# Kernel tuning notes

Measured on AMD Instinct MI355X. Metric: run time of the kernel, lower is better.

Reference implementation:

```python
import jax, jax.numpy as jnp
import numpy as np
import math

B, T, E, F, K, NUM_CONV, H = 32, 2048, 512, 512, 7, 4, 8
EPS = 1e-5


def _ln2(x):
    # fresh nn.LayerNorm(x.size()[1:]): normalize jointly over last two dims, weight=1 bias=0
    mu = jnp.mean(x, axis=(-2, -1), keepdims=True)
    var = jnp.var(x, axis=(-2, -1), keepdims=True)
    return (x - mu) * jax.lax.rsqrt(var + EPS)


def _ds_conv(x, dw_w, dw_b, pw_w, pw_b):
    # x: (B, C, T); depthwise conv (groups=C) then pointwise 1x1
    C = x.shape[1]
    k = dw_w.shape[-1]
    y = jax.lax.conv_general_dilated(
        x, dw_w, window_strides=(1,), padding=[(k // 2, k // 2)],
        dimension_numbers=('NCH', 'OIH', 'NCH'), feature_group_count=C)
    y = y + dw_b[None, :, None]
    y = jnp.einsum('oc,bct->bot', pw_w, y) + pw_b[None, :, None]
    return y


def _pos_enc(n, e):
    # pe[i, 0::2] = sin(i * div), pe[i, 1::2] = cos(i * div); returns (n, 1, e)
    pos = jnp.arange(n, dtype=jnp.float32)[:, None]
    div = jnp.exp(jnp.arange(0, e, 2, dtype=jnp.float32) * (-math.log(10000.0) / e))
    pe = jnp.zeros((n, e), dtype=jnp.float32)
    pe = pe.at[:, 0::2].set(jnp.sin(pos * div)).at[:, 1::2].set(jnp.cos(pos * div))
    return pe[:, None, :]


def setup_inputs() -> dict:
    key = jax.random.key(0)
    ks = jax.random.split(key, 20)
    w = lambda i, shape: (jax.random.normal(ks[i], shape, jnp.float32) * 0.02)
    return {
        'x': jax.random.normal(ks[0], (B, T, E), jnp.float32),
        'dw1_w': w(1, (E, 1, K)), 'dw1_b': w(2, (E,)),
        'pw1_w': w(3, (F, E)), 'pw1_b': w(4, (F,)),
        'dw2_w': w(5, (F, 1, K)), 'dw2_b': w(6, (F,)),
        'pw2_w': w(7, (F, F)), 'pw2_b': w(8, (F,)),
        'wq': w(9, (F, F)), 'bq': w(10, (F,)),
        'wk': w(11, (F, F)), 'bk': w(12, (F,)),
        'wv': w(13, (F, F)), 'bv': w(14, (F,)),
        'wp': w(15, (F, F)), 'bp': w(16, (F,)),
        'ff_w': w(17, (F, F)), 'ff_b': w(18, (F,)),
    }


def reference(x, dw1_w, dw1_b, pw1_w, pw1_b, dw2_w, dw2_b, pw2_w, pw2_b,
              wq, bq, wk, bk, wv, bv, wp, bp, ff_w, ff_b):
    b, t, e = x.shape
    # positional encoding: pe[:x.size(0)] -> (B,1,E), broadcast over T (faithful quirk)
    x = x + _pos_enc(b, e)
    x = jnp.transpose(x, (0, 2, 1))          # (B, E, T)
    x = _ln2(x)
    x = _ds_conv(x, dw1_w, dw1_b, pw1_w, pw1_b)   # (B, F, T)
    for _ in range(NUM_CONV - 1):                 # shared conv weights each iter (faithful)
        x = x + _ds_conv(_ln2(x), dw2_w, dw2_b, pw2_w, pw2_b)
    # attention: code permutes to (T, B, F) so attention attends across the batch axis
    y = jnp.transpose(_ln2(x), (2, 0, 1))    # (T, B, F)
    x = jnp.transpose(x, (2, 0, 1))          # (T, B, F)
    f = x.shape[-1]
    hd = f // H
    q = (y @ wq.T + bq).reshape(t, b, H, hd).transpose(0, 2, 1, 3)  # (T, H, B, hd)
    k = (y @ wk.T + bk).reshape(t, b, H, hd).transpose(0, 2, 1, 3)
    v = (y @ wv.T + bv).reshape(t, b, H, hd).transpose(0, 2, 1, 3)
    att = jnp.einsum('thbd,thcd->thbc', q, k) * (1.0 / math.sqrt(hd))
    att = jax.nn.softmax(att, axis=-1)
    yo = jnp.einsum('thbc,thcd->thbd', att, v)
    yo = yo.transpose(0, 2, 1, 3).reshape(t, b, f)
    yo = yo @ wp.T + bp
    x = x + yo
    y = _ln2(x)                               # norm over last-two dims (B, F)
    y = y @ ff_w.T + ff_b
    x = x + y
    return jnp.transpose(x, (1, 0, 2))        # (B, T, F)
```

## Files before the change

### kernel.cpp

```cpp
#include <hip/hip_runtime.h>
#include <math.h>

constexpr int B_ = 32, T_ = 2048, E_ = 512, F_ = 512, KW = 7, H_ = 8;
constexpr float EPS_ = 1e-5f;

typedef unsigned short bfu;
typedef __attribute__((ext_vector_type(8))) unsigned short ushort8v;
typedef __attribute__((ext_vector_type(8))) short short8v;
typedef __attribute__((ext_vector_type(4))) float f32x4;
typedef const __attribute__((address_space(1))) void* gp1_t;
typedef __attribute__((address_space(3))) void* lp3_t;

__device__ __forceinline__ float b2f(bfu u) {
    return __uint_as_float(((unsigned)u) << 16);
}
__device__ __forceinline__ bfu f2b(float f) {
    unsigned i = __float_as_uint(f);
    i += 0x7fffu + ((i >> 16) & 1u);
    return (bfu)(i >> 16);
}

template <typename T> __device__ __forceinline__ void stv(T* p, size_t i, float v);
template <> __device__ __forceinline__ void stv<bfu>(bfu* p, size_t i, float v)   { p[i] = f2b(v); }
template <> __device__ __forceinline__ void stv<float>(float* p, size_t i, float v) { p[i] = v; }

__global__ void zero_kernel(float* p, int n) {
    int i = blockIdx.x * 256 + threadIdx.x;
    if (i < n) p[i] = 0.f;
}

__global__ void pe_table(float* __restrict__ pe) {
    int i = blockIdx.x * 256 + threadIdx.x;
    int b = i >> 9, e = i & 511;
    float div = expf(-(float)(e & ~1) * (logf(10000.0f) / (float)E_));
    float ang = (float)b * div;
    pe[i] = (e & 1) ? cosf(ang) : sinf(ang);
}

__global__ __launch_bounds__(256) void add_pe(const float* __restrict__ x,
                                              const float* __restrict__ pe,
                                              bfu* __restrict__ out) {
    size_t i = ((size_t)blockIdx.x * 256 + threadIdx.x) * 4;
    int e = (int)(i & 511);
    int b = (int)(i >> 20);
    float4 xv = *(const float4*)(x + i);
    float4 pv = *(const float4*)(pe + (b << 9) + e);
    ushort4 o = { f2b(xv.x + pv.x), f2b(xv.y + pv.y), f2b(xv.z + pv.z), f2b(xv.w + pv.w) };
    *(ushort4*)(out + i) = o;
}

__global__ void w2b(const float* __restrict__ w, bfu* __restrict__ o) {
    int i = (blockIdx.x * 256 + threadIdx.x) * 4;
    float4 v = *(const float4*)(w + i);
    ushort4 u = { f2b(v.x), f2b(v.y), f2b(v.z), f2b(v.w) };
    *(ushort4*)(o + i) = u;
}

__global__ __launch_bounds__(256) void ln_stats(const bfu* __restrict__ x,
                                                float* __restrict__ stats,
                                                int L, int slices) {
    int g = blockIdx.y, s = blockIdx.x;
    int chunk = L / slices;
    const ushort4* p = (const ushort4*)(x + (size_t)g * L + (size_t)s * chunk);
    int n4 = chunk >> 2;
    float sum = 0.f, sq = 0.f;
    for (int i = threadIdx.x; i < n4; i += 256) {
        ushort4 v = p[i];
        float a = b2f(v.x), b = b2f(v.y), c = b2f(v.z), d = b2f(v.w);
        sum += a + b + c + d;
        sq  += a * a + b * b + c * c + d * d;
    }
    #pragma unroll
    for (int off = 32; off > 0; off >>= 1) {
        sum += __shfl_down(sum, off, 64);
        sq  += __shfl_down(sq,  off, 64);
    }
    __shared__ float ss[8];
    int lane = threadIdx.x & 63, wid = threadIdx.x >> 6;
    if (lane == 0) { ss[wid] = sum; ss[4 + wid] = sq; }
    __syncthreads();
    if (threadIdx.x == 0) {
        atomicAdd(&stats[2 * g],     ss[0] + ss[1] + ss[2] + ss[3]);
        atomicAdd(&stats[2 * g + 1], ss[4] + ss[5] + ss[6] + ss[7]);
    }
}

__device__ __forceinline__ float ln_rstd(float sumsq, float mu, float invL) {
    float var = fmaxf(sumsq * invL - mu * mu, 0.f);
    return rsqrtf(var + EPS_);
}

__global__ __launch_bounds__(256) void dwconv_nhwc(const bfu* __restrict__ x,
                                                   const float* __restrict__ stats,
                                                   const float* __restrict__ w,
                                                   const float* __restrict__ bias,
                                                   bfu* __restrict__ out) {
    __shared__ float ws[64 * 57];
    int tid = threadIdx.x;
    int b = blockIdx.z;
    for (int i = tid; i < F_ * KW; i += 256) {
        int f = i / KW, dt = i - f * KW;
        ws[(f >> 3) * 57 + (f & 7) * 7 + dt] = w[i];
    }
    __syncthreads();
    const float invL = 1.0f / (float)(F_ * T_);
    float mu   = stats[2 * b] * invL;
    float rstd = ln_rstd(stats[2 * b + 1], mu, invL);
    int f0 = (tid & 63) * 8;
    int t  = blockIdx.x * 4 + (tid >> 6);
    const bfu* xb = x + (size_t)b * T_ * F_;
    const float* wc_ = &ws[(tid & 63) * 57];
    float acc[8];
    #pragma unroll
    for (int j = 0; j < 8; j++) acc[j] = bias[f0 + j];
    #pragma unroll
    for (int dt = 0; dt < KW; dt++) {
        int tt = t + dt - KW / 2;
        if (tt >= 0 && tt < T_) {
            ushort8v v = *(const ushort8v*)(xb + (size_t)tt * F_ + f0);
            #pragma unroll
            for (int j = 0; j < 8; j++)
                acc[j] += wc_[j * 7 + dt] * ((b2f(v[j]) - mu) * rstd);
        }
    }
    ushort8v o;
    #pragma unroll
    for (int j = 0; j < 8; j++) o[j] = f2b(acc[j]);
    *(ushort8v*)(out + ((size_t)b * T_ + t) * F_ + f0) = o;
}

template <typename OutT>
__global__ __launch_bounds__(256) void gemm_mfma(const bfu* __restrict__ A,
                                                 const bfu* __restrict__ Wb,
                                                 const float* __restrict__ bias,
                                                 const bfu* res, OutT* out,
                                                 int out_transpose) {
    constexpr int Kd = 512;
    __shared__ bfu As[128 * 32];
    __shared__ bfu Bs[128 * 32];
    int id  = blockIdx.x;
    int swz = (id & 7) * 256 + (id >> 3);
    int m0 = (swz & 3) * 128;
    int r0 = (swz >> 2) * 128;
    int tid  = threadIdx.x;
    int wave = tid >> 6, lane = tid & 63;
    int wr = (wave >> 1) * 64, wc = (wave & 1) * 64;
    int lg = lane >> 4,  lr = lane & 15;

    const char* Ab = (const char*)A  + (size_t)r0 * 1024;
    const char* Bb = (const char*)Wb + (size_t)m0 * 1024;
    char* AsB = (char*)As;
    char* BsB = (char*)Bs;
    int rS = (wave << 4) + (lane >> 2);
    int kb = (lane & 3) << 4;
    int ldsoff = wave << 10;

    f32x4 acc[4][4];
    #pragma unroll
    for (int mi = 0; mi < 4; mi++)
        #pragma unroll
        for (int ni = 0; ni < 4; ni++)
            acc[mi][ni] = (f32x4){0.f, 0.f, 0.f, 0.f};

    const bfu* ApL = As + (wr + lr) * 32 + lg * 8;
    const bfu* BpL = Bs + (wc + lr) * 32 + lg * 8;

    for (int k0 = 0; k0 < Kd; k0 += 32) {
        size_t koff = (size_t)(k0 << 1);
        const char* a0 = Ab + (size_t)rS * 1024 + koff + kb;
        const char* b0 = Bb + (size_t)rS * 1024 + koff + kb;
        __builtin_amdgcn_global_load_lds((gp1_t)a0,           (lp3_t)(AsB + ldsoff),        16, 0, 0);
        __builtin_amdgcn_global_load_lds((gp1_t)(a0 + 65536), (lp3_t)(AsB + ldsoff + 4096), 16, 0, 0);
        __builtin_amdgcn_global_load_lds((gp1_t)b0,           (lp3_t)(BsB + ldsoff),        16, 0, 0);
        __builtin_amdgcn_global_load_lds((gp1_t)(b0 + 65536), (lp3_t)(BsB + ldsoff + 4096), 16, 0, 0);
        __syncthreads();
        short8v a[4], bb[4];
        #pragma unroll
        for (int mi = 0; mi < 4; mi++) a[mi]  = *(const short8v*)(ApL + mi * 512);
        #pragma unroll
        for (int ni = 0; ni < 4; ni++) bb[ni] = *(const short8v*)(BpL + ni * 512);
        #pragma unroll
        for (int mi = 0; mi < 4; mi++)
            #pragma unroll
            for (int ni = 0; ni < 4; ni++)
                acc[mi][ni] = __builtin_amdgcn_mfma_f32_16x16x32_bf16(a[mi], bb[ni], acc[mi][ni], 0, 0, 0);
        __syncthreads();
    }

    #pragma unroll
    for (int ni = 0; ni < 4; ni++) {
        int m = m0 + wc + ni * 16 + lr;
        float bv = bias[m];
        #pragma unroll
        for (int mi = 0; mi < 4; mi++) {
            #pragma unroll
            for (int j = 0; j < 4; j++) {
                int r = r0 + wr + mi * 16 + lg * 4 + j;
                float v = acc[mi][ni][j] + bv;
                if (res) v += b2f(res[(size_t)r * 512 + m]);
                if (!out_transpose) {
                    stv(out, (size_t)r * 512 + m, v);
                } else {
                    int t = r >> 5, bb2 = r & 31;
                    stv(out, ((size_t)bb2 * T_ + t) * 512 + m, v);
                }
            }
        }
    }
}

__global__ __launch_bounds__(256) void bt2tb_ln(const bfu* __restrict__ x,
                                                const float* __restrict__ stats,
                                                bfu* __restrict__ xa,
                                                bfu* __restrict__ yln) {
    size_t i = ((size_t)blockIdx.x * 256 + threadIdx.x) * 8;
    int f = (int)(i & 511);
    size_t bt = i >> 9;
    int t = (int)(bt & 2047);
    int b = (int)(bt >> 11);
    const float invL = 1.0f / (float)(F_ * T_);
    float mu   = stats[2 * b] * invL;
    float rstd = ln_rstd(stats[2 * b + 1], mu, invL);
    ushort8v v = *(const ushort8v*)(x + i);
    size_t dst = (((size_t)t * B_ + b) << 9) + f;
    *(ushort8v*)(xa + dst) = v;
    ushort8v o;
    #pragma unroll
    for (int j = 0; j < 8; j++) o[j] = f2b((b2f(v[j]) - mu) * rstd);
    *(ushort8v*)(yln + dst) = o;
}

__global__ __launch_bounds__(256) void ln_apply(const bfu* __restrict__ x,
                                                const float* __restrict__ stats,
                                                bfu* __restrict__ out,
                                                float invL, int shift) {
    size_t i = ((size_t)blockIdx.x * 256 + threadIdx.x) * 8;
    int g = (int)(i >> shift);
    float mu   = stats[2 * g] * invL;
    float rstd = ln_rstd(stats[2 * g + 1], mu, invL);
    ushort8v v = *(const ushort8v*)(x + i);
    ushort8v o;
    #pragma unroll
    for (int j = 0; j < 8; j++) o[j] = f2b((b2f(v[j]) - mu) * rstd);
    *(ushort8v*)(out + i) = o;
}

__global__ __launch_bounds__(256) void attention(const bfu* __restrict__ Q,
                                                 const bfu* __restrict__ K,
                                                 const bfu* __restrict__ V,
                                                 bfu* __restrict__ O) {
    __shared__ float qs[32][65], ks[32][65], vs[32][65], ps[32][33];
    int t = blockIdx.x, h = blockIdx.y;
    int tid = threadIdx.x;
    size_t base = (size_t)t * B_ * F_ + (size_t)h * 64;
    for (int i = tid * 4; i < 32 * 64; i += 1024) {
        int bb = i >> 6, d = i & 63;
        size_t idx = base + (size_t)bb * F_ + d;
        ushort4 q4 = *(const ushort4*)(Q + idx);
        ushort4 k4 = *(const ushort4*)(K + idx);
        ushort4 v4 = *(const ushort4*)(V + idx);
        qs[bb][d] = b2f(q4.x); qs[bb][d + 1] = b2f(q4.y); qs[bb][d + 2] = b2f(q4.z); qs[bb][d + 3] = b2f(q4.w);
        ks[bb][d] = b2f(k4.x); ks[bb][d + 1] = b2f(k4.y); ks[bb][d + 2] = b2f(k4.z); ks[bb][d + 3] = b2f(k4.w);
        vs[bb][d] = b2f(v4.x); vs[bb][d + 1] = b2f(v4.y); vs[bb][d + 2] = b2f(v4.z); vs[bb][d + 3] = b2f(v4.w);
    }
    __syncthreads();
    int brow = tid >> 3;
    int c0   = (tid & 7) * 4;
    float sc0 = 0.f, sc1 = 0.f, sc2 = 0.f, sc3 = 0.f;
    for (int d = 0; d < 64; d++) {
        float qv = qs[brow][d];
        sc0 += qv * ks[c0 + 0][d];
        sc1 += qv * ks[c0 + 1][d];
        sc2 += qv * ks[c0 + 2][d];
        sc3 += qv * ks[c0 + 3][d];
    }
    ps[brow][c0 + 0] = sc0 * 0.125f;
    ps[brow][c0 + 1] = sc1 * 0.125f;
    ps[brow][c0 + 2] = sc2 * 0.125f;
    ps[brow][c0 + 3] = sc3 * 0.125f;
    __syncthreads();
    if (tid < 32) {
        float mx = -1e30f;
        for (int c = 0; c < 32; c++) mx = fmaxf(mx, ps[tid][c]);
        float sum = 0.f;
        for (int c = 0; c < 32; c++) { float e = expf(ps[tid][c] - mx); ps[tid][c] = e; sum += e; }
        float inv = 1.0f / sum;
        for (int c = 0; c < 32; c++) ps[tid][c] *= inv;
    }
    __syncthreads();
    int d0 = (tid & 7) * 8;
    float ov[8] = {};
    for (int c = 0; c < 32; c++) {
        float p = ps[brow][c];
        #pragma unroll
        for (int j = 0; j < 8; j++) ov[j] += p * vs[c][d0 + j];
    }
    #pragma unroll
    for (int j = 0; j < 8; j++)
        O[base + (size_t)brow * F_ + d0 + j] = f2b(ov[j]);
}

extern "C" void kernel_launch(void* const* d_in, const int* in_sizes, int n_in,
                              void* d_out, int out_size, void* d_ws, size_t ws_size,
                              hipStream_t stream) {
    const float* x     = (const float*)d_in[0];
    const float* dw1_w = (const float*)d_in[1];
    const float* dw1_b = (const float*)d_in[2];
    const float* pw1_w = (const float*)d_in[3];
    const float* pw1_b = (const float*)d_in[4];
    const float* dw2_w = (const float*)d_in[5];
    const float* dw2_b = (const float*)d_in[6];
    const float* pw2_w = (const float*)d_in[7];
    const float* pw2_b = (const float*)d_in[8];
    const float* wq = (const float*)d_in[9];   const float* bq = (const float*)d_in[10];
    const float* wk = (const float*)d_in[11];  const float* bk = (const float*)d_in[12];
    const float* wv = (const float*)d_in[13];  const float* bv = (const float*)d_in[14];
    const float* wp = (const float*)d_in[15];  const float* bp = (const float*)d_in[16];
    const float* ffw = (const float*)d_in[17]; const float* ffb = (const float*)d_in[18];
    float* out = (float*)d_out;

    const size_t SZ = (size_t)B_ * F_ * T_;
    const size_t WN = (size_t)F_ * F_;

    float* stats = (float*)d_ws;
    float* peTab = stats + 4096;
    bfu*   wBuf  = (bfu*)(peTab + 16384);
    bfu* wb_pw1 = wBuf + 0 * WN;
    bfu* wb_pw2 = wBuf + 1 * WN;
    bfu* wb_q   = wBuf + 2 * WN;
    bfu* wb_k   = wBuf + 3 * WN;
    bfu* wb_v   = wBuf + 4 * WN;
    bfu* wb_p   = wBuf + 5 * WN;
    bfu* wb_ff  = wBuf + 6 * WN;
    bfu* bufX = (bfu*)d_ws + (1 << 21);
    bfu* bufC = bufX + SZ;
    bfu* bufY = bufC + SZ;
    bfu* bufK = bufY + SZ;
    bfu* bufV = bufK + SZ;

    pe_table<<<64, 256, 0, stream>>>(peTab);
    w2b<<<256, 256, 0, stream>>>(pw1_w, wb_pw1);
    w2b<<<256, 256, 0, stream>>>(pw2_w, wb_pw2);
    w2b<<<256, 256, 0, stream>>>(wq, wb_q);
    w2b<<<256, 256, 0, stream>>>(wk, wb_k);
    w2b<<<256, 256, 0, stream>>>(wv, wb_v);
    w2b<<<256, 256, 0, stream>>>(wp, wb_p);
    w2b<<<256, 256, 0, stream>>>(ffw, wb_ff);
    add_pe<<<32768, 256, 0, stream>>>(x, peTab, bufX);

    auto statsPerB = [&](const bfu* src) {
        zero_kernel<<<16, 256, 0, stream>>>(stats, 4096);
        ln_stats<<<dim3(64, B_), 256, 0, stream>>>(src, stats, F_ * T_, 64);
    };

    statsPerB(bufX);
    dwconv_nhwc<<<dim3(T_ / 4, 1, B_), 256, 0, stream>>>(bufX, stats, dw1_w, dw1_b, bufC);
    gemm_mfma<bfu><<<2048, 256, 0, stream>>>(bufC, wb_pw1, pw1_b, nullptr, bufX, 0);

    for (int it = 0; it < 3; ++it) {
        statsPerB(bufX);
        dwconv_nhwc<<<dim3(T_ / 4, 1, B_), 256, 0, stream>>>(bufX, stats, dw2_w, dw2_b, bufC);
        gemm_mfma<bfu><<<2048, 256, 0, stream>>>(bufC, wb_pw2, pw2_b, bufX, bufX, 0);
    }

    statsPerB(bufX);
    bt2tb_ln<<<16384, 256, 0, stream>>>(bufX, stats, bufC, bufY);

    gemm_mfma<bfu><<<2048, 256, 0, stream>>>(bufY, wb_q, bq, nullptr, bufX, 0);
    gemm_mfma<bfu><<<2048, 256, 0, stream>>>(bufY, wb_k, bk, nullptr, bufK, 0);
    gemm_mfma<bfu><<<2048, 256, 0, stream>>>(bufY, wb_v, bv, nullptr, bufV, 0);

    attention<<<dim3(T_, H_), 256, 0, stream>>>(bufX, bufK, bufV, bufY);

    gemm_mfma<bfu><<<2048, 256, 0, stream>>>(bufY, wb_p, bp, bufC, bufK, 0);

    zero_kernel<<<16, 256, 0, stream>>>(stats, 4096);
    ln_stats<<<dim3(1, T_), 256, 0, stream>>>(bufK, stats, B_ * F_, 1);
    ln_apply<<<16384, 256, 0, stream>>>(bufK, stats, bufX, 1.0f / (float)(B_ * F_), 14);

    gemm_mfma<float><<<2048, 256, 0, stream>>>(bufX, wb_ff, ffb, bufK, out, 1);
}
```

Before: 1.816 ms.

## Fuse LayerNorm stats into GEMM epilogues, MFMA attention, merge prep kernels

Computes the per-batch and per-time LayerNorm sum and sum-of-squares inside the GEMM epilogues and the positional-encoding add, using atomics into pre-zeroed per-stage slots. This removes the separate ln_stats passes and their zeroing launches, so the activations are not re-read for statistics. The attention kernel is rewritten so each wave handles one (t,h) pair, with 32x32x16 bf16 MFMA for QK^T and PV and V transposed through LDS. Weight conversion and PE table generation are merged into one prep kernel. The cost is more atomics and epilogue work in the GEMMs, and statistics that are now accumulated from fp32 values before bf16 rounding.

```diff
diff --git a/kernel.cpp b/kernel.cpp
--- a/kernel.cpp
+++ b/kernel.cpp
@@ -7,7 +7,9 @@
 typedef unsigned short bfu;
 typedef __attribute__((ext_vector_type(8))) unsigned short ushort8v;
 typedef __attribute__((ext_vector_type(8))) short short8v;
+typedef __attribute__((ext_vector_type(4))) short short4v;
 typedef __attribute__((ext_vector_type(4))) float f32x4;
+typedef __attribute__((ext_vector_type(16))) float f32x16;
 typedef const __attribute__((address_space(1))) void* gp1_t;
 typedef __attribute__((address_space(3))) void* lp3_t;
 
@@ -29,46 +31,56 @@
     if (i < n) p[i] = 0.f;
 }
 
-__global__ void pe_table(float* __restrict__ pe) {
-    int i = blockIdx.x * 256 + threadIdx.x;
-    int b = i >> 9, e = i & 511;
-    float div = expf(-(float)(e & ~1) * (logf(10000.0f) / (float)E_));
-    float ang = (float)b * div;
-    pe[i] = (e & 1) ? cosf(ang) : sinf(ang);
+__global__ __launch_bounds__(256) void prep(const float* __restrict__ w0, const float* __restrict__ w1,
+                                            const float* __restrict__ w2, const float* __restrict__ w3,
+                                            const float* __restrict__ w4, const float* __restrict__ w5,
+                                            const float* __restrict__ w6,
+                                            bfu* __restrict__ wb, float* __restrict__ pe) {
+    int idx = blockIdx.x * 256 + threadIdx.x;
+    if (idx < 7 * 65536) {
+        int w = idx >> 16, off = (idx & 65535) * 4;
+        const float* src = w0;
+        switch (w) {
+            case 1: src = w1; break; case 2: src = w2; break; case 3: src = w3; break;
+            case 4: src = w4; break; case 5: src = w5; break; case 6: src = w6; break;
+            default: break;
+        }
+        float4 v = *(const float4*)(src + off);
+        ushort4 u = { f2b(v.x), f2b(v.y), f2b(v.z), f2b(v.w) };
+        *(ushort4*)(wb + (size_t)w * 262144 + off) = u;
+    } else {
+        int i = (idx - 7 * 65536) * 4;
+        if (i < 16384) {
+            #pragma unroll
+            for (int e4 = 0; e4 < 4; e4++) {
+                int ii = i + e4;
+                int b = ii >> 9, e = ii & 511;
+                float div = expf(-(float)(e & ~1) * (logf(10000.0f) / (float)E_));
+                float ang = (float)b * div;
+                pe[ii] = (e & 1) ? cosf(ang) : sinf(ang);
+            }
+        }
+    }
 }
 
 __global__ __launch_bounds__(256) void add_pe(const float* __restrict__ x,
                                               const float* __restrict__ pe,
-                                              bfu* __restrict__ out) {
-    size_t i = ((size_t)blockIdx.x * 256 + threadIdx.x) * 4;
-    int e = (int)(i & 511);
-    int b = (int)(i >> 20);
-    float4 xv = *(const float4*)(x + i);
-    float4 pv = *(const float4*)(pe + (b << 9) + e);
-    ushort4 o = { f2b(xv.x + pv.x), f2b(xv.y + pv.y), f2b(xv.z + pv.z), f2b(xv.w + pv.w) };
-    *(ushort4*)(out + i) = o;
-}
-
-__global__ void w2b(const float* __restrict__ w, bfu* __restrict__ o) {
-    int i = (blockIdx.x * 256 + threadIdx.x) * 4;
-    float4 v = *(const float4*)(w + i);
-    ushort4 u = { f2b(v.x), f2b(v.y), f2b(v.z), f2b(v.w) };
-    *(ushort4*)(o + i) = u;
-}
-
-__global__ __launch_bounds__(256) void ln_stats(const bfu* __restrict__ x,
-                                                float* __restrict__ stats,
-                                                int L, int slices) {
-    int g = blockIdx.y, s = blockIdx.x;
-    int chunk = L / slices;
-    const ushort4* p = (const ushort4*)(x + (size_t)g * L + (size_t)s * chunk);
-    int n4 = chunk >> 2;
+                                              bfu* __restrict__ out,
+                                              float* __restrict__ stats) {
+    size_t base = (size_t)blockIdx.x * 4096;
+    int b = (int)(base >> 20);
     float sum = 0.f, sq = 0.f;
-    for (int i = threadIdx.x; i < n4; i += 256) {
-        ushort4 v = p[i];
-        float a = b2f(v.x), b = b2f(v.y), c = b2f(v.z), d = b2f(v.w);
-        sum += a + b + c + d;
-        sq  += a * a + b * b + c * c + d * d;
+    #pragma unroll
+    for (int u = 0; u < 4; u++) {
+        size_t i = base + u * 1024 + threadIdx.x * 4;
+        int e = (int)(i & 511);
+        float4 xv = *(const float4*)(x + i);
+        float4 pv = *(const float4*)(pe + (b << 9) + e);
+        float a0 = xv.x + pv.x, a1 = xv.y + pv.y, a2 = xv.z + pv.z, a3 = xv.w + pv.w;
+        ushort4 o = { f2b(a0), f2b(a1), f2b(a2), f2b(a3) };
+        *(ushort4*)(out + i) = o;
+        sum += a0 + a1 + a2 + a3;
+        sq  += a0 * a0 + a1 * a1 + a2 * a2 + a3 * a3;
     }
     #pragma unroll
     for (int off = 32; off > 0; off >>= 1) {
@@ -76,12 +88,12 @@
         sq  += __shfl_down(sq,  off, 64);
     }
     __shared__ float ss[8];
-    int lane = threadIdx.x & 63, wid = threadIdx.x >> 6;
-    if (lane == 0) { ss[wid] = sum; ss[4 + wid] = sq; }
+    int lane = threadIdx.x & 63, wv = threadIdx.x >> 6;
+    if (lane == 0) { ss[wv] = sum; ss[4 + wv] = sq; }
     __syncthreads();
     if (threadIdx.x == 0) {
-        atomicAdd(&stats[2 * g],     ss[0] + ss[1] + ss[2] + ss[3]);
-        atomicAdd(&stats[2 * g + 1], ss[4] + ss[5] + ss[6] + ss[7]);
+        atomicAdd(&stats[2 * b],     ss[0] + ss[1] + ss[2] + ss[3]);
+        atomicAdd(&stats[2 * b + 1], ss[4] + ss[5] + ss[6] + ss[7]);
     }
 }
 
@@ -129,12 +141,12 @@
     *(ushort8v*)(out + ((size_t)b * T_ + t) * F_ + f0) = o;
 }
 
-template <typename OutT>
+template <typename OutT, int GMODE>
 __global__ __launch_bounds__(256) void gemm_mfma(const bfu* __restrict__ A,
                                                  const bfu* __restrict__ Wb,
                                                  const float* __restrict__ bias,
                                                  const bfu* res, OutT* out,
-                                                 int out_transpose) {
+                                                 int out_transpose, float* stats) {
     constexpr int Kd = 512;
     __shared__ bfu As[128 * 32];
     __shared__ bfu Bs[128 * 32];
@@ -187,6 +199,7 @@
         __syncthreads();
     }
 
+    float sAcc0 = 0.f, sAcc1 = 0.f, qAcc0 = 0.f, qAcc1 = 0.f;
     #pragma unroll
     for (int ni = 0; ni < 4; ni++) {
         int m = m0 + wc + ni * 16 + lr;
@@ -198,6 +211,10 @@
                 int r = r0 + wr + mi * 16 + lg * 4 + j;
                 float v = acc[mi][ni][j] + bv;
                 if (res) v += b2f(res[(size_t)r * 512 + m]);
+                if (GMODE) {
+                    if (mi < 2) { sAcc0 += v; qAcc0 += v * v; }
+                    else        { sAcc1 += v; qAcc1 += v * v; }
+                }
                 if (!out_transpose) {
                     stv(out, (size_t)r * 512 + m, v);
                 } else {
@@ -205,6 +222,32 @@
                     stv(out, ((size_t)bb2 * T_ + t) * 512 + m, v);
                 }
             }
+        }
+    }
+    if (GMODE == 1) {
+        float s = sAcc0 + sAcc1, q = qAcc0 + qAcc1;
+        #pragma unroll
+        for (int off = 32; off > 0; off >>= 1) {
+            s += __shfl_down(s, off, 64);
+            q += __shfl_down(q, off, 64);
+        }
+        if (lane == 0) {
+            int g = r0 >> 11;
+            atomicAdd(&stats[2 * g], s);
+            atomicAdd(&stats[2 * g + 1], q);
+        }
+    } else if (GMODE == 2) {
+        #pragma unroll
+        for (int off = 32; off > 0; off >>= 1) {
+            sAcc0 += __shfl_down(sAcc0, off, 64); qAcc0 += __shfl_down(qAcc0, off, 64);
+            sAcc1 += __shfl_down(sAcc1, off, 64); qAcc1 += __shfl_down(qAcc1, off, 64);
+        }
+        if (lane == 0) {
+            int g0 = (r0 >> 5) + (wr >> 5);
+            atomicAdd(&stats[2 * g0],     sAcc0);
+            atomicAdd(&stats[2 * g0 + 1], qAcc0);
+            atomicAdd(&stats[2 * g0 + 2], sAcc1);
+            atomicAdd(&stats[2 * g0 + 3], qAcc1);
         }
     }
 }
@@ -245,59 +288,87 @@
     *(ushort8v*)(out + i) = o;
 }
 
-__global__ __launch_bounds__(256) void attention(const bfu* __restrict__ Q,
-                                                 const bfu* __restrict__ K,
-                                                 const bfu* __restrict__ V,
-                                                 bfu* __restrict__ O) {
-    __shared__ float qs[32][65], ks[32][65], vs[32][65], ps[32][33];
-    int t = blockIdx.x, h = blockIdx.y;
+__global__ __launch_bounds__(256) void attention_mfma(const bfu* __restrict__ Q,
+                                                      const bfu* __restrict__ K,
+                                                      const bfu* __restrict__ V,
+                                                      bfu* __restrict__ O) {
+    __shared__ bfu vt[4][64 * 36];
     int tid = threadIdx.x;
-    size_t base = (size_t)t * B_ * F_ + (size_t)h * 64;
-    for (int i = tid * 4; i < 32 * 64; i += 1024) {
-        int bb = i >> 6, d = i & 63;
-        size_t idx = base + (size_t)bb * F_ + d;
-        ushort4 q4 = *(const ushort4*)(Q + idx);
-        ushort4 k4 = *(const ushort4*)(K + idx);
-        ushort4 v4 = *(const ushort4*)(V + idx);
-        qs[bb][d] = b2f(q4.x); qs[bb][d + 1] = b2f(q4.y); qs[bb][d + 2] = b2f(q4.z); qs[bb][d + 3] = b2f(q4.w);
-        ks[bb][d] = b2f(k4.x); ks[bb][d + 1] = b2f(k4.y); ks[bb][d + 2] = b2f(k4.z); ks[bb][d + 3] = b2f(k4.w);
-        vs[bb][d] = b2f(v4.x); vs[bb][d + 1] = b2f(v4.y); vs[bb][d + 2] = b2f(v4.z); vs[bb][d + 3] = b2f(v4.w);
-    }
-    __syncthreads();
-    int brow = tid >> 3;
-    int c0   = (tid & 7) * 4;
-    float sc0 = 0.f, sc1 = 0.f, sc2 = 0.f, sc3 = 0.f;
-    for (int d = 0; d < 64; d++) {
-        float qv = qs[brow][d];
-        sc0 += qv * ks[c0 + 0][d];
-        sc1 += qv * ks[c0 + 1][d];
-        sc2 += qv * ks[c0 + 2][d];
-        sc3 += qv * ks[c0 + 3][d];
-    }
-    ps[brow][c0 + 0] = sc0 * 0.125f;
-    ps[brow][c0 + 1] = sc1 * 0.125f;
-    ps[brow][c0 + 2] = sc2 * 0.125f;
-    ps[brow][c0 + 3] = sc3 * 0.125f;
-    __syncthreads();
-    if (tid < 32) {
-        float mx = -1e30f;
-        for (int c = 0; c < 32; c++) mx = fmaxf(mx, ps[tid][c]);
-        float sum = 0.f;
-        for (int c = 0; c < 32; c++) { float e = expf(ps[tid][c] - mx); ps[tid][c] = e; sum += e; }
-        float inv = 1.0f / sum;
-        for (int c = 0; c < 32; c++) ps[tid][c] *= inv;
-    }
-    __syncthreads();
-    int d0 = (tid & 7) * 8;
-    float ov[8] = {};
-    for (int c = 0; c < 32; c++) {
-        float p = ps[brow][c];
-        #pragma unroll
-        for (int j = 0; j < 8; j++) ov[j] += p * vs[c][d0 + j];
-    }
-    #pragma unroll
-    for (int j = 0; j < 8; j++)
-        O[base + (size_t)brow * F_ + d0 + j] = f2b(ov[j]);
+    int wave = tid >> 6, lane = tid & 63;
+    int wid = blockIdx.x * 4 + wave;
+    int t = wid >> 3, h = wid & 7;
+    int lh = lane >> 5, lm = lane & 31;
+    size_t base = (size_t)t * (B_ * F_) + (size_t)h * 64;
+
+    short8v qf[4], kf[4];
+    const bfu* qrow = Q + base + (size_t)lm * F_ + lh * 8;
+    const bfu* krow = K + base + (size_t)lm * F_ + lh * 8;
+    #pragma unroll
+    for (int s = 0; s < 4; s++) {
+        qf[s] = *(const short8v*)(qrow + s * 16);
+        kf[s] = *(const short8v*)(krow + s * 16);
+    }
+    bfu* vt_w = vt[wave];
+    {
+        int c = lane >> 1, d0 = (lane & 1) * 32;
+        const bfu* vrow = V + base + (size_t)c * F_ + d0;
+        #pragma unroll
+        for (int j = 0; j < 4; j++) {
+            ushort8v vv = *(const ushort8v*)(vrow + j * 8);
+            #pragma unroll
+            for (int e = 0; e < 8; e++)
+                vt_w[(d0 + j * 8 + e) * 36 + c] = vv[e];
+        }
+    }
+    f32x16 st;
+    #pragma unroll
+    for (int r = 0; r < 16; r++) st[r] = 0.f;
+    #pragma unroll
+    for (int s = 0; s < 4; s++)
+        st = __builtin_amdgcn_mfma_f32_32x32x16_bf16(kf[s], qf[s], st, 0, 0, 0);
+
+    float p[16];
+    float mx = -1e30f;
+    #pragma unroll
+    for (int r = 0; r < 16; r++) { p[r] = st[r] * 0.125f; mx = fmaxf(mx, p[r]); }
+    mx = fmaxf(mx, __shfl_xor(mx, 32, 64));
+    float sum = 0.f;
+    #pragma unroll
+    for (int r = 0; r < 16; r++) { p[r] = expf(p[r] - mx); sum += p[r]; }
+    sum += __shfl_xor(sum, 32, 64);
+    float inv = 1.0f / sum;
+    short8v pa[2];
+    #pragma unroll
+    for (int j = 0; j < 8; j++) {
+        pa[0][j] = (short)f2b(p[j] * inv);
+        pa[1][j] = (short)f2b(p[8 + j] * inv);
+    }
+    f32x16 oacc[2];
+    #pragma unroll
+    for (int dt = 0; dt < 2; dt++)
+        #pragma unroll
+        for (int r = 0; r < 16; r++) oacc[dt][r] = 0.f;
+    #pragma unroll
+    for (int dt = 0; dt < 2; dt++) {
+        const bfu* vr = vt_w + (dt * 32 + lm) * 36 + lh * 4;
+        #pragma unroll
+        for (int kh = 0; kh < 2; kh++) {
+            short4v b0 = *(const short4v*)(vr + kh * 16);
+            short4v b1 = *(const short4v*)(vr + kh * 16 + 8);
+            short8v bf;
+            #pragma unroll
+            for (int e = 0; e < 4; e++) { bf[e] = b0[e]; bf[4 + e] = b1[e]; }
+            oacc[dt] = __builtin_amdgcn_mfma_f32_32x32x16_bf16(pa[kh], bf, oacc[dt], 0, 0, 0);
+        }
+    }
+    bfu* orow = O + base + lm;
+    #pragma unroll
+    for (int dt = 0; dt < 2; dt++)
+        #pragma unroll
+        for (int r = 0; r < 16; r++) {
+            int b = (r & 3) + 8 * (r >> 2) + 4 * lh;
+            orow[(size_t)b * F_ + dt * 32] = f2b(oacc[dt][r]);
+        }
 }
 
 extern "C" void kernel_launch(void* const* d_in, const int* in_sizes, int n_in,
@@ -323,7 +394,13 @@
     const size_t WN = (size_t)F_ * F_;
 
     float* stats = (float*)d_ws;
-    float* peTab = stats + 4096;
+    float* stA = stats;
+    float* st1 = stats + 128;
+    float* st2 = stats + 256;
+    float* st3 = stats + 384;
+    float* st4 = stats + 512;
+    float* stT = stats + 1024;
+    float* peTab = stats + 8192;
     bfu*   wBuf  = (bfu*)(peTab + 16384);
     bfu* wb_pw1 = wBuf + 0 * WN;
     bfu* wb_pw2 = wBuf + 1 * WN;
@@ -338,45 +415,31 @@
     bfu* bufK = bufY + SZ;
     bfu* bufV = bufK + SZ;
 
-    pe_table<<<64, 256, 0, stream>>>(peTab);
-    w2b<<<256, 256, 0, stream>>>(pw1_w, wb_pw1);
-    w2b<<<256, 256, 0, stream>>>(pw2_w, wb_pw2);
-    w2b<<<256, 256, 0, stream>>>(wq, wb_q);
-    w2b<<<256, 256, 0, stream>>>(wk, wb_k);
-    w2b<<<256, 256, 0, stream>>>(wv, wb_v);
-    w2b<<<256, 256, 0, stream>>>(wp, wb_p);
-    w2b<<<256, 256, 0, stream>>>(ffw, wb_ff);
-    add_pe<<<32768, 256, 0, stream>>>(x, peTab, bufX);
-
-    auto statsPerB = [&](const bfu* src) {
-        zero_kernel<<<16, 256, 0, stream>>>(stats, 4096);
-        ln_stats<<<dim3(64, B_), 256, 0, stream>>>(src, stats, F_ * T_, 64);
-    };
-
-    statsPerB(bufX);
-    dwconv_nhwc<<<dim3(T_ / 4, 1, B_), 256, 0, stream>>>(bufX, stats, dw1_w, dw1_b, bufC);
-    gemm_mfma<bfu><<<2048, 256, 0, stream>>>(bufC, wb_pw1, pw1_b, nullptr, bufX, 0);
-
+    zero_kernel<<<32, 256, 0, stream>>>(stats, 8192);
+    prep<<<1808, 256, 0, stream>>>(pw1_w, pw2_w, wq, wk, wv, wp, ffw, wBuf, peTab);
+    add_pe<<<8192, 256, 0, stream>>>(x, peTab, bufX, stA);
+
+    dwconv_nhwc<<<dim3(T_ / 4, 1, B_), 256, 0, stream>>>(bufX, stA, dw1_w, dw1_b, bufC);
+    gemm_mfma<bfu, 1><<<2048, 256, 0, stream>>>(bufC, wb_pw1, pw1_b, nullptr, bufX, 0, st1);
+
+    float* sts[3] = { st2, st3, st4 };
     for (int it = 0; it < 3; ++it) {
-        statsPerB(bufX);
-        dwconv_nhwc<<<dim3(T_ / 4, 1, B_), 256, 0, stream>>>(bufX, stats, dw2_w, dw2_b, bufC);
-        gemm_mfma<bfu><<<2048, 256, 0, stream>>>(bufC, wb_pw2, pw2_b, bufX, bufX, 0);
-    }
-
-    statsPerB(bufX);
-    bt2tb_ln<<<16384, 256, 0, stream>>>(bufX, stats, bufC, bufY);
-
-    gemm_mfma<bfu><<<2048, 256, 0, stream>>>(bufY, wb_q, bq, nullptr, bufX, 0);
-    gemm_mfma<bfu><<<2048, 256, 0, stream>>>(bufY, wb_k, bk, nullptr, bufK, 0);
-    gemm_mfma<bfu><<<2048, 256, 0, stream>>>(bufY, wb_v, bv, nullptr, bufV, 0);
-
-    attention<<<dim3(T_, H_), 256, 0, stream>>>(bufX, bufK, bufV, bufY);
-
-    gemm_mfma<bfu><<<2048, 256, 0, stream>>>(bufY, wb_p, bp, bufC, bufK, 0);
-
-    zero_kernel<<<16, 256, 0, stream>>>(stats, 4096);
-    ln_stats<<<dim3(1, T_), 256, 0, stream>>>(bufK, stats, B_ * F_, 1);
-    ln_apply<<<16384, 256, 0, stream>>>(bufK, stats, bufX, 1.0f / (float)(B_ * F_), 14);
-
-    gemm_mfma<float><<<2048, 256, 0, stream>>>(bufX, wb_ff, ffb, bufK, out, 1);
-}
+        float* sin_ = (it == 0) ? st1 : sts[it - 1];
+        dwconv_nhwc<<<dim3(T_ / 4, 1, B_), 256, 0, stream>>>(bufX, sin_, dw2_w, dw2_b, bufC);
+        gemm_mfma<bfu, 1><<<2048, 256, 0, stream>>>(bufC, wb_pw2, pw2_b, bufX, bufX, 0, sts[it]);
+    }
+
+    bt2tb_ln<<<16384, 256, 0, stream>>>(bufX, st4, bufC, bufY);
+
+    gemm_mfma<bfu, 0><<<2048, 256, 0, stream>>>(bufY, wb_q, bq, nullptr, bufX, 0, nullptr);
+    gemm_mfma<bfu, 0><<<2048, 256, 0, stream>>>(bufY, wb_k, bk, nullptr, bufK, 0, nullptr);
+    gemm_mfma<bfu, 0><<<2048, 256, 0, stream>>>(bufY, wb_v, bv, nullptr, bufV, 0, nullptr);
+
+    attention_mfma<<<4096, 256, 0, stream>>>(bufX, bufK, bufV, bufY);
+
+    gemm_mfma<bfu, 2><<<2048, 256, 0, stream>>>(bufY, wb_p, bp, bufC, bufK, 0, stT);
+
+    ln_apply<<<16384, 256, 0, stream>>>(bufK, stT, bufX, 1.0f / (float)(B_ * F_), 14);
+
+    gemm_mfma<float, 0><<<2048, 256, 0, stream>>>(bufX, wb_ff, ffb, bufK, out, 1, nullptr);
+}
```

Measured after the change: 1.825 ms. No clear change (+0.5%).
